# Performance work log

Measured on AMD Instinct MI355X. Metric: run time of the kernel, lower is better.

Reference implementation:

```python
import jax, jax.numpy as jnp
import numpy as np

# ---- architecture constants ----
SENSOR = 128          # u feature width
B_LAYERS = 5          # branch MLP: 4 tanh hidden + 1 linear out
B_UNITS = 1024
LORA = 64
TU = 128              # trunk hidden units
TL = 4                # trunk dense layers
TRUNK_DIMS = [1] + [TU] * (TL - 1) + [1]   # 1 -> 128 -> 128 -> 128 -> 1
NO_TRUNK_PARAMS = sum(d_out + d_in * d_out for d_in, d_out in zip(TRUNK_DIMS[:-1], TRUNK_DIMS[1:]))  # 33409
T0, TFINAL = 0.0, 1.0
BATCH = 2048


def setup_inputs() -> dict:
    key = jax.random.key(0)
    ks = jax.random.split(key, 16)
    def glorot(k, shape):
        fan_in, fan_out = shape[0], shape[1]
        s = jnp.sqrt(2.0 / (fan_in + fan_out)).astype(jnp.float32)
        return jax.random.normal(k, shape, dtype=jnp.float32) * s
    inp = {
        "t": jax.random.uniform(ks[0], (BATCH, 1), dtype=jnp.float32),
        "u": jax.random.normal(ks[1], (BATCH, SENSOR), dtype=jnp.float32),
        # branch MLP: Dense(1024)+tanh x4, then Dense(1024)
        "bw0": glorot(ks[2], (SENSOR, B_UNITS)), "bb0": jnp.zeros((B_UNITS,), jnp.float32),
        "bw1": glorot(ks[3], (B_UNITS, B_UNITS)), "bb1": jnp.zeros((B_UNITS,), jnp.float32),
        "bw2": glorot(ks[4], (B_UNITS, B_UNITS)), "bb2": jnp.zeros((B_UNITS,), jnp.float32),
        "bw3": glorot(ks[5], (B_UNITS, B_UNITS)), "bb3": jnp.zeros((B_UNITS,), jnp.float32),
        "bw4": glorot(ks[6], (B_UNITS, B_UNITS)), "bb4": jnp.zeros((B_UNITS,), jnp.float32),
        # LoRA factors generating trunk params
        "W1": glorot(ks[7], (B_UNITS, LORA)),
        "W2": glorot(ks[8], (LORA, NO_TRUNK_PARAMS)),
    }
    return inp


def _slice_trunk(p):
    """Split per-sample flat trunk params [B,P] into (kernel,bias) per layer.
    Flax tree_flatten order per Dense: bias then kernel."""
    layers = []
    k = 0
    for d_in, d_out in zip(TRUNK_DIMS[:-1], TRUNK_DIMS[1:]):
        b = p[:, k:k + d_out]; k += d_out
        W = p[:, k:k + d_in * d_out].reshape(-1, d_in, d_out); k += d_in * d_out
        layers.append((W, b))
    return layers


def reference(t, u, bw0, bb0, bw1, bb1, bw2, bb2, bw3, bb3, bw4, bb4, W1, W2):
    q0 = u[:, :1]                                     # [B,1]
    # branch MLP (hypernetwork body)
    net = u
    for W, b in ((bw0, bb0), (bw1, bb1), (bw2, bb2), (bw3, bb3)):
        net = jnp.tanh(net @ W + b)
    net = net @ bw4 + bb4                             # [B, units]
    # LoRA-generated per-sample trunk params
    params = net @ (W1 @ W2)                          # [B, NO_TRUNK_PARAMS]
    # batched per-sample trunk MLP on t[i] (vectorized form of the Python loop)
    x = t                                             # [B,1]
    trunk_layers = _slice_trunk(params)
    for i, (W, b) in enumerate(trunk_layers):
        x = jnp.einsum('bi,bio->bo', x, W) + b
        if i < TL - 1:
            x = jnp.tanh(x)
    q = x                                             # [B,1]
    # hard constraint: u0 + (t-t0)/(tfinal-t0)*nn
    out = q0 + (t - T0) / (TFINAL - T0) * q           # [B,1]
    return out.reshape(-1)
```

## Files before the change

kernel.cpp:

```cpp
#include <hip/hip_runtime.h>
#include <hip/hip_bf16.h>
#include <stdint.h>

typedef unsigned short u16;
typedef unsigned int   u32;
typedef short s16x8 __attribute__((ext_vector_type(8)));
typedef float f32x4 __attribute__((ext_vector_type(4)));

#define LDP 33409

__device__ __forceinline__ u16 f2bf(float f) {
    union { float f; u32 u; } v; v.f = f;
    u32 r = v.u + 0x7fffu + ((v.u >> 16) & 1u);
    return (u16)(r >> 16);
}
__device__ __forceinline__ float bf2f(u16 h) {
    union { u32 u; float f; } v; v.u = ((u32)h) << 16;
    return v.f;
}
__device__ __forceinline__ float fast_tanh(float x) {
    float e = __expf(2.0f * x);
    return 1.0f - 2.0f / (e + 1.0f);
}
__device__ __forceinline__ f32x4 MFMA(s16x8 a, s16x8 b, f32x4 c) {
    return __builtin_amdgcn_mfma_f32_16x16x32_bf16(a, b, c, 0, 0, 0);
}
__device__ __forceinline__ void gload_lds16(const void* g, void* l) {
    __builtin_amdgcn_global_load_lds(
        (const __attribute__((address_space(1))) u32*)(uintptr_t)g,
        (__attribute__((address_space(3))) u32*)(uintptr_t)l, 16, 0, 0);
}

__global__ __launch_bounds__(256)
void prep0(const float* __restrict__ u, const float* __restrict__ bw0,
           u16* __restrict__ ubf, u16* __restrict__ bw0t)
{
    __shared__ float tile[64][65];
    const int bid = blockIdx.x, tid = threadIdx.x;
    if (bid < 128) {
        int i = (bid * 256 + tid) * 8;
        float4 a = *(const float4*)&u[i];
        float4 b = *(const float4*)&u[i + 4];
        uint4 o;
        o.x = (u32)f2bf(a.x) | ((u32)f2bf(a.y) << 16);
        o.y = (u32)f2bf(a.z) | ((u32)f2bf(a.w) << 16);
        o.z = (u32)f2bf(b.x) | ((u32)f2bf(b.y) << 16);
        o.w = (u32)f2bf(b.z) | ((u32)f2bf(b.w) << 16);
        *(uint4*)&ubf[i] = o;
        return;
    }
    const int idx = bid - 128;
    const int rb = (idx >> 4) * 64, cb = (idx & 15) * 64;
    for (int i = tid; i < 64 * 64; i += 256) {
        int r = i >> 6, c = i & 63;
        tile[r][c] = bw0[(size_t)(rb + r) * 1024 + cb + c];
    }
    __syncthreads();
    for (int i = tid; i < 64 * 64; i += 256) {
        int c = i >> 6, r = i & 63;
        bw0t[(size_t)(cb + c) * 128 + rb + r] = f2bf(tile[r][c]);
    }
}

__global__ __launch_bounds__(256, 2)
void gemm_fused(const u16* __restrict__ A, int lda,
                const u16* __restrict__ Bt, int ldb,
                const float* __restrict__ bias,
                u16* __restrict__ Cout, int ldc, int K, int mode,
                const float* __restrict__ xsrc, u16* __restrict__ xdst,
                const float* __restrict__ bw4, const float* __restrict__ bb4,
                const float* __restrict__ W1, u16* __restrict__ BWt,
                float* __restrict__ bz,
                const float* __restrict__ W2, u16* __restrict__ Btb)
{
    __shared__ __align__(16) char lds[24576];
    const int bid = blockIdx.x, tid = threadIdx.x;

    if (bid < 256) {
        u16 (*As)[128 * 32] = (u16(*)[128 * 32])lds;
        u16 (*Bs)[64 * 32]  = (u16(*)[64 * 32])(lds + 16384);
        const int lane = tid & 63, wid = tid >> 6;
        const int wr = wid >> 1, wc = wid & 1;
        const int bn = (bid & 15) * 64, bm = (bid >> 4) * 128;
        const int NT = K >> 5;
        const int arow = tid >> 2, ck = tid & 3;
        const u16* aSrc = A + (size_t)(bm + arow) * lda + (ck ^ (arow & 3)) * 8;
        const u16* bSrc = Bt + (size_t)(bn + arow) * ldb + (ck ^ (arow & 3)) * 8;
        const size_t aHalf = (size_t)64 * lda;
        f32x4 acc[4][2] = {};

        auto STAGE = [&](int buf, int t) {
            const int k0 = t << 5;
            gload_lds16(aSrc + k0,         (char*)As[buf] + wid * 1024);
            gload_lds16(aSrc + aHalf + k0, (char*)As[buf] + 4096 + wid * 1024);
            gload_lds16(bSrc + k0,         (char*)Bs[buf] + wid * 1024);
        };
        auto COMPUTE = [&](int buf) {
            s16x8 av[4], bv[2];
            #pragma unroll
            for (int mi = 0; mi < 4; ++mi) {
                int row = wr * 64 + mi * 16 + (lane & 15);
                int s = (lane >> 4) ^ (row & 3);
                av[mi] = *(const s16x8*)&As[buf][row * 32 + s * 8];
            }
            #pragma unroll
            for (int ni = 0; ni < 2; ++ni) {
                int col = wc * 32 + ni * 16 + (lane & 15);
                int s = (lane >> 4) ^ (col & 3);
                bv[ni] = *(const s16x8*)&Bs[buf][col * 32 + s * 8];
            }
            #pragma unroll
            for (int mi = 0; mi < 4; ++mi)
            #pragma unroll
            for (int ni = 0; ni < 2; ++ni)
                acc[mi][ni] = MFMA(av[mi], bv[ni], acc[mi][ni]);
        };

        STAGE(0, 0);
        __syncthreads();
        for (int t = 0; t < NT; ++t) {
            if (t + 1 < NT) STAGE((t + 1) & 1, t + 1);
            COMPUTE(t & 1);
            __syncthreads();
        }
        #pragma unroll
        for (int mi = 0; mi < 4; ++mi)
        #pragma unroll
        for (int ni = 0; ni < 2; ++ni) {
            const int col = bn + wc * 32 + ni * 16 + (lane & 15);
            const float bv = bias[col];
            #pragma unroll
            for (int jj = 0; jj < 4; ++jj) {
                const int row = bm + wr * 64 + mi * 16 + (lane >> 4) * 4 + jj;
                Cout[(size_t)row * ldc + col] = f2bf(fast_tanh(acc[mi][ni][jj] + bv));
            }
        }
    } else if (mode <= 2 && bid < 512) {
        float (*tile)[65] = (float(*)[65])lds;
        const int idx = bid - 256;
        const int rb = (idx >> 4) * 64, cb = (idx & 15) * 64;
        for (int i = tid; i < 64 * 64; i += 256) {
            int r = i >> 6, c = i & 63;
            tile[r][c] = xsrc[(size_t)(rb + r) * 1024 + cb + c];
        }
        __syncthreads();
        for (int i = tid; i < 64 * 64; i += 256) {
            int c = i >> 6, r = i & 63;
            xdst[(size_t)(cb + c) * 1024 + rb + r] = f2bf(tile[r][c]);
        }
    } else if (mode == 2) {
        const int lb = bid - 512;
        const int n = tid & 63, jc = tid >> 6;
        if (lb == 512) {
            float (*sh1)[64] = (float(*)[64])lds;
            float a = 0.f;
            for (int j = jc * 256; j < jc * 256 + 256; ++j)
                a = fmaf(bb4[j], W1[j * 64 + n], a);
            sh1[jc][n] = a;
            __syncthreads();
            if (tid < 64)
                bz[tid] = sh1[0][tid] + sh1[1][tid] + sh1[2][tid] + sh1[3][tid];
            return;
        }
        float (*sh)[2][64] = (float(*)[2][64])lds;
        const int k0 = lb * 2;
        float a0 = 0.f, a1 = 0.f;
        for (int j = jc * 256; j < jc * 256 + 256; ++j) {
            float w = W1[j * 64 + n];
            a0 = fmaf(bw4[(size_t)k0 * 1024 + j], w, a0);
            a1 = fmaf(bw4[(size_t)(k0 + 1) * 1024 + j], w, a1);
        }
        sh[jc][0][n] = a0; sh[jc][1][n] = a1;
        __syncthreads();
        if (tid < 128) {
            int kk = tid >> 6, nn = tid & 63;
            float s = sh[0][kk][nn] + sh[1][kk][nn] + sh[2][kk][nn] + sh[3][kk][nn];
            BWt[(size_t)nn * 1024 + k0 + kk] = f2bf(s);
        }
    } else {
        float (*tile)[130] = (float(*)[130])lds;
        const int idx = bid - 256;
        const int layer = idx / 258, pbi = idx % 258;
        u16* Btd = Btb + (size_t)layer * 128 * 8256;
        const int colbase = layer ? 16896 : 384, biasbase = layer ? 16768 : 256;
        const int pb = pbi * 32;
        for (int i = tid; i < 32 * 128; i += 256) {
            int p = pb + (i >> 7), n = i & 127;
            float v = (p < 8192)
                ? W2[(size_t)(p & 63) * LDP + colbase + (size_t)(p >> 6) * 128 + n]
                : W2[(size_t)(p - 8192) * LDP + biasbase + n];
            tile[i >> 7][n] = v;
        }
        __syncthreads();
        for (int i = tid; i < 32 * 128; i += 256) {
            int n = i >> 5, dp = i & 31;
            Btd[(size_t)n * 8256 + pb + dp] = f2bf(tile[dp][n]);
        }
    }
}

__global__ __launch_bounds__(256, 2)
void zgemm(const u16* __restrict__ A, const u16* __restrict__ Bt,
           float* __restrict__ zc)
{
    __shared__ __align__(16) u16 As[2][64 * 32];
    __shared__ __align__(16) u16 Bs[2][64 * 32];
    const int tid = threadIdx.x, lane = tid & 63, wid = tid >> 6;
    const int wr = wid >> 1, wc = wid & 1;
    const int bm = blockIdx.y * 64, kz = blockIdx.z;
    const int t0 = kz * 4, nt = 4;
    const int arow = tid >> 2, ck = tid & 3;
    const u16* aSrc = A + (size_t)(bm + arow) * 1024 + (ck ^ (arow & 3)) * 8;
    const u16* bSrc = Bt + (size_t)arow * 1024 + (ck ^ (arow & 3)) * 8;
    f32x4 acc[2][2] = {};

    auto STAGE = [&](int buf, int t) {
        const int k0 = t << 5;
        gload_lds16(aSrc + k0, (char*)As[buf] + wid * 1024);
        gload_lds16(bSrc + k0, (char*)Bs[buf] + wid * 1024);
    };
    auto COMPUTE = [&](int buf) {
        s16x8 a[2];
        #pragma unroll
        for (int mi = 0; mi < 2; ++mi) {
            int row = wr * 32 + mi * 16 + (lane & 15);
            int s = (lane >> 4) ^ (row & 3);
            a[mi] = *(const s16x8*)&As[buf][row * 32 + s * 8];
        }
        #pragma unroll
        for (int ni = 0; ni < 2; ++ni) {
            int n = wc * 32 + ni * 16 + (lane & 15);
            int s = (lane >> 4) ^ (n & 3);
            s16x8 b = *(const s16x8*)&Bs[buf][n * 32 + s * 8];
            #pragma unroll
            for (int mi = 0; mi < 2; ++mi)
                acc[mi][ni] = MFMA(a[mi], b, acc[mi][ni]);
        }
    };

    STAGE(0, t0);
    __syncthreads();
    for (int t = 0; t < nt; ++t) {
        if (t + 1 < nt) STAGE((t + 1) & 1, t0 + t + 1);
        COMPUTE(t & 1);
        __syncthreads();
    }
    #pragma unroll
    for (int mi = 0; mi < 2; ++mi)
    #pragma unroll
    for (int ni = 0; ni < 2; ++ni) {
        const int col = wc * 32 + ni * 16 + (lane & 15);
        #pragma unroll
        for (int jj = 0; jj < 4; ++jj) {
            const int row = bm + wr * 32 + mi * 16 + (lane >> 4) * 4 + jj;
            zc[((size_t)kz * 2048 + row) * 64 + col] = acc[mi][ni][jj];
        }
    }
}

__global__ __launch_bounds__(256)
void z_l1_h1(const float* __restrict__ zc, const float* __restrict__ bz,
             const float* __restrict__ W2, const float* __restrict__ t,
             u16* __restrict__ z, u16* __restrict__ h1)
{
    __shared__ float zsh[16][64];
    const int rb = blockIdx.x * 16;
    #pragma unroll
    for (int ii = 0; ii < 4; ++ii) {
        int e = ii * 256 + threadIdx.x;
        int r = e >> 6, k = e & 63;
        size_t off = (size_t)(rb + r) * 64 + k;
        float s = bz[k];
        #pragma unroll
        for (int sk = 0; sk < 8; ++sk) s += zc[(size_t)sk * 2048 * 64 + off];
        zsh[r][k] = s;
        z[off] = f2bf(s);
    }
    __syncthreads();
    const int o = threadIdx.x & 127;
    const int rh = (threadIdx.x >> 7) * 8;
    float acc_a[8] = {}, acc_b[8] = {};
    for (int k = 0; k < 64; ++k) {
        float wa = W2[(size_t)k * LDP + o];
        float wb = W2[(size_t)k * LDP + 128 + o];
        #pragma unroll
        for (int r = 0; r < 8; ++r) {
            float zv = zsh[rh + r][k];
            acc_a[r] = fmaf(zv, wa, acc_a[r]);
            acc_b[r] = fmaf(zv, wb, acc_b[r]);
        }
    }
    #pragma unroll
    for (int r = 0; r < 8; ++r) {
        int b = rb + rh + r;
        h1[b * 128 + o] = f2bf(fast_tanh(t[b] * acc_b[r] + acc_a[r]));
    }
}

__global__ __launch_bounds__(512, 2)
void trunk128(const u16* __restrict__ h, const u16* __restrict__ z,
              const u16* __restrict__ Bt, float* __restrict__ Cp)
{
    constexpr int NT = 258, SKT = 16;
    __shared__ __align__(16) u16 As[2][128 * 32];
    __shared__ __align__(16) u16 Bs[2][128 * 32];
    const int tid = threadIdx.x, lane = tid & 63, wid = tid >> 6;
    const int wr = wid >> 1, wc = wid & 1;
    const int bm = blockIdx.x * 128, kz = blockIdx.y;
    const int t0 = (NT * kz) / SKT, t1 = (NT * (kz + 1)) / SKT;
    const int arow = tid >> 2, ck = tid & 3;
    const int b = bm + arow;
    const s16x8 zlo = *(const s16x8*)&z[b * 64 + ck * 8];
    const s16x8 zhi = *(const s16x8*)&z[b * 64 + 32 + ck * 8];
    const int slot = (ck ^ (arow & 3)) * 8;
    f32x4 acc[2][4] = {};

    auto STAGE = [&](int buf, int t) {
        const int p0 = t << 5;
        gload_lds16(Bt + (size_t)arow * 8256 + p0 + (ck ^ (arow & 3)) * 8,
                    (char*)Bs[buf] + wid * 1024);
        const s16x8 zv = (p0 & 32) ? zhi : zlo;
        u16 o8[8];
        if (p0 < 8192) {
            const float hf = bf2f(h[b * 128 + (p0 >> 6)]);
            #pragma unroll
            for (int j = 0; j < 8; ++j) o8[j] = f2bf(hf * bf2f((u16)zv[j]));
        } else {
            #pragma unroll
            for (int j = 0; j < 8; ++j) o8[j] = (u16)zv[j];
        }
        *(s16x8*)&As[buf][arow * 32 + slot] = *(s16x8*)o8;
    };
    auto COMPUTE = [&](int buf) {
        s16x8 av[2], bb[4];
        #pragma unroll
        for (int mi = 0; mi < 2; ++mi) {
            int row = wr * 32 + mi * 16 + (lane & 15);
            int s = (lane >> 4) ^ (row & 3);
            av[mi] = *(const s16x8*)&As[buf][row * 32 + s * 8];
        }
        #pragma unroll
        for (int ni = 0; ni < 4; ++ni) {
            int n = wc * 64 + ni * 16 + (lane & 15);
            int s = (lane >> 4) ^ (n & 3);
            bb[ni] = *(const s16x8*)&Bs[buf][n * 32 + s * 8];
        }
        #pragma unroll
        for (int mi = 0; mi < 2; ++mi)
        #pragma unroll
        for (int ni = 0; ni < 4; ++ni)
            acc[mi][ni] = MFMA(av[mi], bb[ni], acc[mi][ni]);
    };

    STAGE(0, t0);
    __syncthreads();
    const int nt = t1 - t0;
    for (int t = 0; t < nt; ++t) {
        if (t + 1 < nt) STAGE((t + 1) & 1, t0 + t + 1);
        COMPUTE(t & 1);
        __syncthreads();
    }

    #pragma unroll
    for (int mi = 0; mi < 2; ++mi)
    #pragma unroll
    for (int ni = 0; ni < 4; ++ni) {
        const int col = wc * 64 + ni * 16 + (lane & 15);
        #pragma unroll
        for (int jj = 0; jj < 4; ++jj) {
            const int row = bm + wr * 32 + mi * 16 + (lane >> 4) * 4 + jj;
            Cp[((size_t)kz * 2048 + row) * 128 + col] = acc[mi][ni][jj];
        }
    }
}

__global__ __launch_bounds__(256)
void reduce_tanh(const float* __restrict__ Cp, u16* __restrict__ hout) {
    const int i4 = (blockIdx.x * 256 + threadIdx.x) * 4;
    const size_t S = (size_t)2048 * 128;
    float4 s = make_float4(0.f, 0.f, 0.f, 0.f);
    #pragma unroll
    for (int k = 0; k < 16; ++k) {
        float4 v = *(const float4*)&Cp[(size_t)k * S + i4];
        s.x += v.x; s.y += v.y; s.z += v.z; s.w += v.w;
    }
    uint2 o;
    o.x = (u32)f2bf(fast_tanh(s.x)) | ((u32)f2bf(fast_tanh(s.y)) << 16);
    o.y = (u32)f2bf(fast_tanh(s.z)) | ((u32)f2bf(fast_tanh(s.w)) << 16);
    *(uint2*)&hout[i4] = o;
}

__global__ __launch_bounds__(256)
void reduce_out(const float* __restrict__ Cp, const u16* __restrict__ z,
                const float* __restrict__ W2, const float* __restrict__ t,
                const float* __restrict__ u, float* __restrict__ out)
{
    __shared__ float sh[4][128];
    const int wv = threadIdx.x >> 6, l = threadIdx.x & 63;
    const int b = blockIdx.x * 4 + wv;
    const size_t S = (size_t)2048 * 128;
    #pragma unroll
    for (int e = l; e < 128; e += 64) {
        float s = 0.f;
        #pragma unroll
        for (int k = 0; k < 16; ++k) s += Cp[k * S + (size_t)b * 128 + e];
        sh[wv][e] = fast_tanh(s);
    }
    __syncthreads();
    const float* wrow = &W2[(size_t)l * LDP + 33280];
    float acc = wrow[0];
    #pragma unroll 8
    for (int i = 0; i < 128; ++i) acc = fmaf(sh[wv][i], wrow[1 + i], acc);
    float p = bf2f(z[b * 64 + l]) * acc;
    #pragma unroll
    for (int off = 32; off > 0; off >>= 1) p += __shfl_down(p, off);
    if (l == 0) out[b] = u[b * 128] + t[b] * p;
}

extern "C" void kernel_launch(void* const* d_in, const int* in_sizes, int n_in,
                              void* d_out, int out_size, void* d_ws, size_t ws_size,
                              hipStream_t stream)
{
    const float* t   = (const float*)d_in[0];
    const float* u   = (const float*)d_in[1];
    const float* bw0 = (const float*)d_in[2];
    const float* bb0 = (const float*)d_in[3];
    const float* bw1 = (const float*)d_in[4];
    const float* bb1 = (const float*)d_in[5];
    const float* bw2 = (const float*)d_in[6];
    const float* bb2 = (const float*)d_in[7];
    const float* bw3 = (const float*)d_in[8];
    const float* bb3 = (const float*)d_in[9];
    const float* bw4 = (const float*)d_in[10];
    const float* bb4 = (const float*)d_in[11];
    const float* W1  = (const float*)d_in[12];
    const float* W2  = (const float*)d_in[13];
    float* out = (float*)d_out;

    char* base = (char*)d_ws;
    u16*   bw1t = (u16*)(base);
    u16*   bw2t = (u16*)(base + 2097152);
    u16*   bw3t = (u16*)(base + 4194304);
    u16*   actA = (u16*)(base + 6291456);
    u16*   actB = (u16*)(base + 10485760);
    u16*   ubf  = (u16*)(base + 14680064);
    u16*   bw0t = (u16*)(base + 15204352);
    u16*   BWt  = (u16*)(base + 15499264);
    float* bz   = (float*)(base + 15630336);
    u16*   z    = (u16*)(base + 16777216);
    u16*   h1   = (u16*)(base + 17039360);
    u16*   h2   = (u16*)(base + 17563648);
    u16*   Bt   = (u16*)(base + 18087936);
    float* zc = (float*)(base);
    float* Cp = (float*)(base);

    dim3 blk(256);
    prep0<<<160, blk, 0, stream>>>(u, bw0, ubf, bw0t);

    gemm_fused<<<512, blk, 0, stream>>>(
        ubf, 128, bw0t, 128, bb0, actA, 1024, 128, 0,
        bw1, bw1t, bw4, bb4, W1, BWt, bz, W2, Bt);
    gemm_fused<<<512, blk, 0, stream>>>(
        actA, 1024, bw1t, 1024, bb1, actB, 1024, 1024, 1,
        bw2, bw2t, bw4, bb4, W1, BWt, bz, W2, Bt);
    gemm_fused<<<1025, blk, 0, stream>>>(
        actB, 1024, bw2t, 1024, bb2, actA, 1024, 1024, 2,
        bw3, bw3t, bw4, bb4, W1, BWt, bz, W2, Bt);
    gemm_fused<<<772, blk, 0, stream>>>(
        actA, 1024, bw3t, 1024, bb3, actB, 1024, 1024, 3,
        nullptr, nullptr, bw4, bb4, W1, BWt, bz, W2, Bt);
    zgemm<<<dim3(1, 32, 8), blk, 0, stream>>>(actB, BWt, zc);
    z_l1_h1<<<128, blk, 0, stream>>>(zc, bz, W2, t, z, h1);
    trunk128<<<dim3(16, 16), dim3(512), 0, stream>>>(h1, z, Bt, Cp);
    reduce_tanh<<<256, blk, 0, stream>>>(Cp, h2);
    trunk128<<<dim3(16, 16), dim3(512), 0, stream>>>(h2, z, Bt + (size_t)128 * 8256, Cp);
    reduce_out<<<512, blk, 0, stream>>>(Cp, z, W2, t, u, out);
}
```

Before: 137.9 us.

## Fuse fp32-to-bf16 conversion and bw0 transpose into layer-0 GEMM loader

Replaces the separate prep0 kernel and the first gemm_fused launch with a single gemm_l0 kernel. It reads fp32 u and bw0 directly, converts them to bf16 while staging into swizzled LDS, and transposes bw0 on the fly. Extra blocks in the same launch transpose bw1. This removes one kernel launch and the intermediate ubf/bw0t round-trip through global memory, at the cost of strided scalar LDS stores for B. The trunk128 grid index mapping also swaps x/y so the split-K index varies fastest, which changes block scheduling order.

```diff
diff --git a/kernel.cpp b/kernel.cpp
--- a/kernel.cpp
+++ b/kernel.cpp
@@ -31,34 +31,103 @@
         (__attribute__((address_space(3))) u32*)(uintptr_t)l, 16, 0, 0);
 }
 
-__global__ __launch_bounds__(256)
-void prep0(const float* __restrict__ u, const float* __restrict__ bw0,
-           u16* __restrict__ ubf, u16* __restrict__ bw0t)
-{
-    __shared__ float tile[64][65];
+__global__ __launch_bounds__(256, 2)
+void gemm_l0(const float* __restrict__ u, const float* __restrict__ bw0,
+             const float* __restrict__ bias, u16* __restrict__ Cout,
+             const float* __restrict__ bw1, u16* __restrict__ bw1t)
+{
+    __shared__ __align__(16) char lds[24576];
     const int bid = blockIdx.x, tid = threadIdx.x;
-    if (bid < 128) {
-        int i = (bid * 256 + tid) * 8;
-        float4 a = *(const float4*)&u[i];
-        float4 b = *(const float4*)&u[i + 4];
-        uint4 o;
-        o.x = (u32)f2bf(a.x) | ((u32)f2bf(a.y) << 16);
-        o.y = (u32)f2bf(a.z) | ((u32)f2bf(a.w) << 16);
-        o.z = (u32)f2bf(b.x) | ((u32)f2bf(b.y) << 16);
-        o.w = (u32)f2bf(b.z) | ((u32)f2bf(b.w) << 16);
-        *(uint4*)&ubf[i] = o;
-        return;
-    }
-    const int idx = bid - 128;
-    const int rb = (idx >> 4) * 64, cb = (idx & 15) * 64;
-    for (int i = tid; i < 64 * 64; i += 256) {
-        int r = i >> 6, c = i & 63;
-        tile[r][c] = bw0[(size_t)(rb + r) * 1024 + cb + c];
-    }
-    __syncthreads();
-    for (int i = tid; i < 64 * 64; i += 256) {
-        int c = i >> 6, r = i & 63;
-        bw0t[(size_t)(cb + c) * 128 + rb + r] = f2bf(tile[r][c]);
+
+    if (bid < 256) {
+        u16 (*As)[128 * 32] = (u16(*)[128 * 32])lds;
+        u16 (*Bs)[64 * 32]  = (u16(*)[64 * 32])(lds + 16384);
+        const int lane = tid & 63, wid = tid >> 6;
+        const int wr = wid >> 1, wc = wid & 1;
+        const int bn = (bid & 15) * 64, bm = (bid >> 4) * 128;
+        f32x4 acc[4][2] = {};
+
+        auto STAGE = [&](int buf, int t) {
+            const int k0 = t << 5;
+            #pragma unroll
+            for (int r = 0; r < 2; ++r) {
+                int idx = r * 256 + tid;
+                int row = idx >> 2, ck = idx & 3;
+                const float* src = u + (size_t)(bm + row) * 128 + k0 + ck * 8;
+                float4 x = *(const float4*)src;
+                float4 y = *(const float4*)(src + 4);
+                u16 o8[8] = {f2bf(x.x), f2bf(x.y), f2bf(x.z), f2bf(x.w),
+                             f2bf(y.x), f2bf(y.y), f2bf(y.z), f2bf(y.w)};
+                *(s16x8*)&As[buf][row * 32 + ((ck ^ (row & 3)) << 3)] = *(s16x8*)o8;
+            }
+            {
+                int kk = tid >> 3, cg = tid & 7;
+                const float* src = bw0 + (size_t)(k0 + kk) * 1024 + bn + cg * 8;
+                float4 x = *(const float4*)src;
+                float4 y = *(const float4*)(src + 4);
+                float v[8] = {x.x, x.y, x.z, x.w, y.x, y.y, y.z, y.w};
+                const int c = kk >> 3, e = kk & 7;
+                #pragma unroll
+                for (int j = 0; j < 8; ++j) {
+                    int col = cg * 8 + j;
+                    Bs[buf][col * 32 + ((c ^ (col & 3)) << 3) + e] = f2bf(v[j]);
+                }
+            }
+        };
+        auto COMPUTE = [&](int buf) {
+            s16x8 av[4], bv[2];
+            #pragma unroll
+            for (int mi = 0; mi < 4; ++mi) {
+                int row = wr * 64 + mi * 16 + (lane & 15);
+                int s = (lane >> 4) ^ (row & 3);
+                av[mi] = *(const s16x8*)&As[buf][row * 32 + s * 8];
+            }
+            #pragma unroll
+            for (int ni = 0; ni < 2; ++ni) {
+                int col = wc * 32 + ni * 16 + (lane & 15);
+                int s = (lane >> 4) ^ (col & 3);
+                bv[ni] = *(const s16x8*)&Bs[buf][col * 32 + s * 8];
+            }
+            #pragma unroll
+            for (int mi = 0; mi < 4; ++mi)
+            #pragma unroll
+            for (int ni = 0; ni < 2; ++ni)
+                acc[mi][ni] = MFMA(av[mi], bv[ni], acc[mi][ni]);
+        };
+
+        STAGE(0, 0);
+        __syncthreads();
+        #pragma unroll
+        for (int t = 0; t < 4; ++t) {
+            if (t + 1 < 4) STAGE((t + 1) & 1, t + 1);
+            COMPUTE(t & 1);
+            __syncthreads();
+        }
+        #pragma unroll
+        for (int mi = 0; mi < 4; ++mi)
+        #pragma unroll
+        for (int ni = 0; ni < 2; ++ni) {
+            const int col = bn + wc * 32 + ni * 16 + (lane & 15);
+            const float bv = bias[col];
+            #pragma unroll
+            for (int jj = 0; jj < 4; ++jj) {
+                const int row = bm + wr * 64 + mi * 16 + (lane >> 4) * 4 + jj;
+                Cout[(size_t)row * 1024 + col] = f2bf(fast_tanh(acc[mi][ni][jj] + bv));
+            }
+        }
+    } else {
+        float (*tile)[65] = (float(*)[65])lds;
+        const int idx = bid - 256;
+        const int rb = (idx >> 4) * 64, cb = (idx & 15) * 64;
+        for (int i = tid; i < 64 * 64; i += 256) {
+            int r = i >> 6, c = i & 63;
+            tile[r][c] = bw1[(size_t)(rb + r) * 1024 + cb + c];
+        }
+        __syncthreads();
+        for (int i = tid; i < 64 * 64; i += 256) {
+            int c = i >> 6, r = i & 63;
+            bw1t[(size_t)(cb + c) * 1024 + rb + r] = f2bf(tile[r][c]);
+        }
     }
 }
 
@@ -306,7 +375,7 @@
     __shared__ __align__(16) u16 Bs[2][128 * 32];
     const int tid = threadIdx.x, lane = tid & 63, wid = tid >> 6;
     const int wr = wid >> 1, wc = wid & 1;
-    const int bm = blockIdx.x * 128, kz = blockIdx.y;
+    const int bm = blockIdx.y * 128, kz = blockIdx.x;
     const int t0 = (NT * kz) / SKT, t1 = (NT * (kz + 1)) / SKT;
     const int arow = tid >> 2, ck = tid & 3;
     const int b = bm + arow;
@@ -443,8 +512,6 @@
     u16*   bw3t = (u16*)(base + 4194304);
     u16*   actA = (u16*)(base + 6291456);
     u16*   actB = (u16*)(base + 10485760);
-    u16*   ubf  = (u16*)(base + 14680064);
-    u16*   bw0t = (u16*)(base + 15204352);
     u16*   BWt  = (u16*)(base + 15499264);
     float* bz   = (float*)(base + 15630336);
     u16*   z    = (u16*)(base + 16777216);
@@ -455,11 +522,7 @@
     float* Cp = (float*)(base);
 
     dim3 blk(256);
-    prep0<<<160, blk, 0, stream>>>(u, bw0, ubf, bw0t);
-
-    gemm_fused<<<512, blk, 0, stream>>>(
-        ubf, 128, bw0t, 128, bb0, actA, 1024, 128, 0,
-        bw1, bw1t, bw4, bb4, W1, BWt, bz, W2, Bt);
+    gemm_l0<<<512, blk, 0, stream>>>(u, bw0, bb0, actA, bw1, bw1t);
     gemm_fused<<<512, blk, 0, stream>>>(
         actA, 1024, bw1t, 1024, bb1, actB, 1024, 1024, 1,
         bw2, bw2t, bw4, bb4, W1, BWt, bz, W2, Bt);
```

New measurement: 139.4 us. Within noise of the previous version (+1.1%).
